# Performance work log

Hardware: AMD Instinct MI355X
Metric: run time of the kernel (lower is better)

Reference implementation:

```python
import jax, jax.numpy as jnp
import numpy as np

EPS = 1e-6
NUM_HEADS = 16

def _feature_map(x):
    # elu(x) + 1
    return jnp.where(x > 0, x + 1.0, jnp.exp(x))

def setup_inputs() -> dict:
    key = jax.random.key(0)
    ks = jax.random.split(key, 7)
    B, L, S, D = 4, 4096, 4096, 2048
    sc = 1.0 / np.sqrt(D)
    return {
        "query": jax.random.normal(ks[0], (B, L, D), jnp.float32),
        "kv": jax.random.normal(ks[1], (B, S, D), jnp.float32),
        "Wq": jax.random.normal(ks[2], (D, D), jnp.float32) * sc,
        "Wg": jax.random.normal(ks[3], (D, D), jnp.float32) * sc,
        "bg": jnp.ones((D,), jnp.float32),
        "Wkv": jax.random.normal(ks[4], (2 * D, D), jnp.float32) * sc,
        "Wo": jax.random.normal(ks[5], (D, D), jnp.float32) * sc,
    }

def reference(query, kv, Wq, Wg, bg, Wkv, Wo):
    B, L, D = query.shape
    S = kv.shape[1]
    H = NUM_HEADS
    hd = D // H
    q = query @ Wq.T                      # [B,L,D]
    gate = jax.nn.sigmoid(query @ Wg.T + bg)  # [B,L,D]
    kvp = kv @ Wkv.T                      # [B,S,2D]
    k, v = jnp.split(kvp, 2, axis=-1)
    # reshape to heads: [B,H,L,hd]
    q = _feature_map(q.reshape(B, L, H, hd).transpose(0, 2, 1, 3))
    k = _feature_map(k.reshape(B, S, H, hd).transpose(0, 2, 1, 3))
    v = v.reshape(B, S, H, hd).transpose(0, 2, 1, 3)
    kv_summary = jnp.einsum('bhsd,bhse->bhde', k, v)   # [B,H,hd,hd]
    k_sum = k.sum(axis=-2)                              # [B,H,hd]
    z = 1.0 / (jnp.einsum('bhld,bhd->bhl', q, k_sum)[..., None] + EPS)
    attn = jnp.einsum('bhld,bhde->bhle', q, kv_summary) * z  # [B,H,L,hd]
    attn = attn.transpose(0, 2, 1, 3).reshape(B, L, D)
    out = (attn * gate) @ Wo.T
    return out
```

## Files before the change

kernel.cpp:

```cpp
#include <hip/hip_runtime.h>

typedef __attribute__((ext_vector_type(8))) short bf16x8;
typedef __attribute__((ext_vector_type(4))) float f32x4;
typedef __attribute__((ext_vector_type(4))) unsigned int u32x4;

constexpr int L_ = 4096, S_ = 4096, D_ = 2048, H_ = 16, HD_ = 128;
constexpr int LDSS = 72;

__device__ __forceinline__ unsigned short f2bf(float f) {
    unsigned int u = __builtin_bit_cast(unsigned int, f);
    return (unsigned short)((u + 0x7fffu + ((u >> 16) & 1u)) >> 16);
}
__device__ __forceinline__ float bf2f(unsigned short h) {
    unsigned int u = ((unsigned int)h) << 16;
    return __builtin_bit_cast(float, u);
}
__device__ __forceinline__ unsigned long long pack4(float a, float b, float c, float d) {
    return (unsigned long long)f2bf(a) | ((unsigned long long)f2bf(b) << 16)
         | ((unsigned long long)f2bf(c) << 32) | ((unsigned long long)f2bf(d) << 48);
}
__device__ __forceinline__ float featmap(float x) {
    return x > 0.f ? x + 1.f : __expf(x);
}
__device__ __forceinline__ void gload16(const unsigned short* g, unsigned short* l) {
    __builtin_amdgcn_global_load_lds(
        (const __attribute__((address_space(1))) void*)g,
        (__attribute__((address_space(3))) void*)l, 16, 0, 0);
}

__global__ __launch_bounds__(256) void cvt_bf16(
    const float* __restrict__ in, unsigned short* __restrict__ out, int n8)
{
    const int stride = gridDim.x * 256;
    for (int i = blockIdx.x * 256 + threadIdx.x; i < n8; i += stride) {
        const float4 a = ((const float4*)in)[2 * i];
        const float4 b = ((const float4*)in)[2 * i + 1];
        unsigned long long* o = (unsigned long long*)&out[(size_t)i * 8];
        o[0] = pack4(a.x, a.y, a.z, a.w);
        o[1] = pack4(b.x, b.y, b.z, b.w);
    }
}

template<int MODE, int NBN>
__global__ __launch_bounds__(512, 2) void gemm256(
    const unsigned short* __restrict__ A, const unsigned short* __restrict__ B,
    unsigned short* __restrict__ C1, unsigned short* __restrict__ C2,
    float* __restrict__ Cf, const float* __restrict__ bias)
{
    __shared__ alignas(16) unsigned short lds[65536];
    const int tid = threadIdx.x;
    const int lane = tid & 63, w = tid >> 6;
    const int wr = w >> 2, wc = w & 3;
    const int lr = lane & 15;
    const int lk8 = (lane >> 4) * 8;
    const int rsw = (lr & 7) << 3;
    const int lsub = lane >> 3;
    const int scol = ((lane & 7) ^ lsub) * 8;

    const int nwg = gridDim.x;
    const int wg = blockIdx.x;
    const int swz = (wg & 7) * (nwg >> 3) + (wg >> 3);
    const int bm = swz / NBN, bn = swz % NBN;
    const int row0 = bm * 256, bcol = bn * 256;

    const unsigned short* Ap = A + (size_t)row0 * D_;
    const unsigned short* Bp = B + (size_t)bcol * D_;
    const int rA = w * 8 + lsub;
    const int rB = ((w * 8 + lsub) >> 5) * 64 + ((w * 8 + lsub) & 31);

    f32x4 acc[8][4] = {};
    bf16x8 av[2][4], bv[2][4];

#define STA(BUF, HH, KT) do { \
    const unsigned short* g_ = Ap + (size_t)((HH) * 64 + rA) * D_ + (KT) * 64 + scol; \
    unsigned short* l_ = &lds[(BUF) * 16384 + (HH) * 8192 + w * 512]; \
    gload16(g_, l_); gload16(g_ + (size_t)128 * D_, l_ + 4096); } while (0)

#define STB(BUF, HH, KT) do { \
    const unsigned short* g_ = Bp + (size_t)(rB + (HH) * 32) * D_ + (KT) * 64 + scol; \
    unsigned short* l_ = &lds[32768 + (BUF) * 16384 + (HH) * 8192 + w * 512]; \
    gload16(g_, l_); gload16(g_ + (size_t)128 * D_, l_ + 4096); } while (0)

#define RD_A(MQ, BUF) \
    _Pragma("unroll") for (int mi = 0; mi < 4; mi++) \
    _Pragma("unroll") for (int ks = 0; ks < 2; ks++) \
        av[ks][mi] = *(const bf16x8*)&lds[(BUF) * 16384 + (MQ) * 8192 \
            + (mi * 16 + lr + wr * 64) * 64 + ((ks * 32 + lk8) ^ rsw)];

#define RD_B(NQ, BUF) \
    _Pragma("unroll") for (int j = 0; j < 2; j++) \
    _Pragma("unroll") for (int ks = 0; ks < 2; ks++) \
        bv[ks][(NQ) * 2 + j] = *(const bf16x8*)&lds[32768 + (BUF) * 16384 + (NQ) * 8192 \
            + (j * 16 + lr + wc * 32) * 64 + ((ks * 32 + lk8) ^ rsw)];

#define MFMA_Q(MQ, NQ) \
    __builtin_amdgcn_s_setprio(1); \
    _Pragma("unroll") for (int mi = 0; mi < 4; mi++) \
    _Pragma("unroll") for (int j = 0; j < 2; j++) \
    _Pragma("unroll") for (int ks = 0; ks < 2; ks++) \
        acc[(MQ) * 4 + mi][(NQ) * 2 + j] = __builtin_amdgcn_mfma_f32_16x16x32_bf16( \
            av[ks][mi], bv[ks][(NQ) * 2 + j], acc[(MQ) * 4 + mi][(NQ) * 2 + j], 0, 0, 0); \
    __builtin_amdgcn_s_setprio(0);

#define BAR __builtin_amdgcn_s_barrier()
#define LGKM do { asm volatile("s_waitcnt lgkmcnt(0)" ::: "memory"); \
                  __builtin_amdgcn_sched_barrier(0); } while (0)
#define VM6 asm volatile("s_waitcnt vmcnt(6)" ::: "memory")
#define VM0 asm volatile("s_waitcnt vmcnt(0)" ::: "memory")

    STA(0, 0, 0); STB(0, 0, 0); STB(0, 1, 0); STA(0, 1, 0);
    STA(1, 0, 1); STB(1, 0, 1); STB(1, 1, 1);
    VM6;
    BAR;

    constexpr int NT = D_ / 64;
    for (int i = 0; i < NT / 2 - 1; i++) {
        const int T = 2 * i;
        RD_A(0, 0); RD_B(0, 0); STA(1, 1, T + 1);
        BAR; LGKM; MFMA_Q(0, 0); BAR;
        RD_B(1, 0); STA(0, 0, T + 2);
        BAR; LGKM; MFMA_Q(0, 1); BAR;
        RD_A(1, 0); STB(0, 0, T + 2);
        BAR; LGKM; MFMA_Q(1, 0); BAR;
        STB(0, 1, T + 2);
        VM6; BAR; MFMA_Q(1, 1); BAR;
        RD_A(0, 1); RD_B(0, 1); STA(0, 1, T + 2);
        BAR; LGKM; MFMA_Q(0, 0); BAR;
        RD_B(1, 1); STA(1, 0, T + 3);
        BAR; LGKM; MFMA_Q(0, 1); BAR;
        RD_A(1, 1); STB(1, 0, T + 3);
        BAR; LGKM; MFMA_Q(1, 0); BAR;
        STB(1, 1, T + 3);
        VM6; BAR; MFMA_Q(1, 1); BAR;
    }
    {
        RD_A(0, 0); RD_B(0, 0); STA(1, 1, NT - 1);
        BAR; LGKM; MFMA_Q(0, 0); BAR;
        RD_B(1, 0);
        BAR; LGKM; MFMA_Q(0, 1); BAR;
        RD_A(1, 0);
        BAR; LGKM; MFMA_Q(1, 0); BAR;
        VM0; BAR; MFMA_Q(1, 1); BAR;
        RD_A(0, 1); RD_B(0, 1);
        BAR; LGKM; MFMA_Q(0, 0); BAR;
        RD_B(1, 1);
        BAR; LGKM; MFMA_Q(0, 1); BAR;
        RD_A(1, 1);
        BAR; LGKM; MFMA_Q(1, 0); BAR;
        BAR; MFMA_Q(1, 1); BAR;
    }

    const int rb = (lane >> 4) * 4;
    const bool second = bn >= (NBN / 2);
    if (MODE == 1) {
        unsigned short* TT = lds;
        const int b = row0 >> 12;
        #pragma unroll
        for (int qd = 0; qd < 4; qd++) {
            const int sq = qd >> 1, dh = qd & 1;
            __syncthreads();
            if (wr == sq && (wc >> 1) == dh) {
                #pragma unroll
                for (int m = 0; m < 8; m++) {
                    #pragma unroll
                    for (int n = 0; n < 4; n++) {
                        float x0 = acc[m][n][0], x1 = acc[m][n][1];
                        float x2 = acc[m][n][2], x3 = acc[m][n][3];
                        if (!second) {
                            x0 = featmap(x0); x1 = featmap(x1);
                            x2 = featmap(x2); x3 = featmap(x3);
                        }
                        const int dcol = (wc & 1) * 64 + n * 16 + lr;
                        *(unsigned long long*)&TT[dcol * 136 + m * 16 + rb]
                            = pack4(x0, x1, x2, x3);
                    }
                }
            }
            __syncthreads();
            const int h2 = (bn & 7) * 2 + dh;
            const int s0 = (row0 + sq * 128) & (S_ - 1);
            unsigned short* dst = (second ? C2 : C1) + (size_t)(b * H_ + h2) * HD_ * S_;
            #pragma unroll
            for (int it = 0; it < 4; it++) {
                const int idx = it * 512 + tid;
                const int d = idx >> 4, sc2 = (idx & 15) * 8;
                *(u32x4*)&dst[(size_t)d * S_ + s0 + sc2] = *(const u32x4*)&TT[d * 136 + sc2];
            }
        }
        return;
    }
    #pragma unroll
    for (int m = 0; m < 8; m++) {
        #pragma unroll
        for (int n = 0; n < 4; n++) {
            #pragma unroll
            for (int r = 0; r < 4; r++) {
                const size_t gr = (size_t)(row0 + wr * 128 + m * 16 + rb + r);
                const int gc = bcol + wc * 64 + n * 16 + lr;
                float x = acc[m][n][r];
                if (MODE == 0) {
                    if (!second) {
                        C1[gr * D_ + gc] = f2bf(featmap(x));
                    } else {
                        const int gc2 = gc - D_;
                        float t = x + bias[gc2];
                        C2[gr * D_ + gc2] = f2bf(1.f / (1.f + __expf(-t)));
                    }
                } else {
                    Cf[gr * D_ + gc] = x;
                }
            }
        }
    }
#undef STA
#undef STB
#undef RD_A
#undef RD_B
#undef MFMA_Q
#undef BAR
#undef LGKM
#undef VM6
#undef VM0
}

__global__ __launch_bounds__(256) void kvsum_part(
    const unsigned short* __restrict__ kT, const unsigned short* __restrict__ vT,
    float* __restrict__ part, float* __restrict__ ksum_part)
{
    __shared__ unsigned short kA[HD_ * LDSS];
    __shared__ unsigned short vB[HD_ * LDSS];
    __shared__ float red[HD_ * 8];
    const int tid = threadIdx.x;
    const int cx = blockIdx.x, bh = blockIdx.y;
    const int lane = tid & 63, w = tid >> 6;
    const int wm = (w >> 1) * 64, wn = (w & 1) * 64;
    const int lr = lane & 15, lk = (lane >> 4) * 8;
    const unsigned short* kb = kT + (size_t)bh * HD_ * S_;
    const unsigned short* vb = vT + (size_t)bh * HD_ * S_;
    f32x4 acc[4][4] = {};
    float ksl[4] = {0.f, 0.f, 0.f, 0.f};
    const int chunk = S_ / 8;
    const int s_begin = cx * chunk;
    for (int s0 = s_begin; s0 < s_begin + chunk; s0 += 64) {
        #pragma unroll
        for (int i = 0; i < 4; i++) {
            int idx = tid + i * 256;
            int d = idx >> 3, sc = (idx & 7) * 8;
            u32x4 kk = *(const u32x4*)&kb[(size_t)d * S_ + s0 + sc];
            *(u32x4*)&kA[d * LDSS + sc] = kk;
            unsigned short t8[8];
            *(u32x4*)t8 = kk;
            float ss = 0.f;
            #pragma unroll
            for (int j = 0; j < 8; j++) ss += bf2f(t8[j]);
            ksl[i] += ss;
            *(u32x4*)&vB[d * LDSS + sc] = *(const u32x4*)&vb[(size_t)d * S_ + s0 + sc];
        }
        __syncthreads();
        #pragma unroll
        for (int ks = 0; ks < 64; ks += 32) {
            bf16x8 av[4], bv[4];
            #pragma unroll
            for (int mi = 0; mi < 4; mi++)
                av[mi] = *(const bf16x8*)&kA[(wm + mi * 16 + lr) * LDSS + ks + lk];
            #pragma unroll
            for (int ni = 0; ni < 4; ni++)
                bv[ni] = *(const bf16x8*)&vB[(wn + ni * 16 + lr) * LDSS + ks + lk];
            #pragma unroll
            for (int mi = 0; mi < 4; mi++)
                #pragma unroll
                for (int ni = 0; ni < 4; ni++)
                    acc[mi][ni] = __builtin_amdgcn_mfma_f32_16x16x32_bf16(
                        av[mi], bv[ni], acc[mi][ni], 0, 0, 0);
        }
        __syncthreads();
    }
    #pragma unroll
    for (int i = 0; i < 4; i++) red[((tid >> 3) + 32 * i) * 8 + (tid & 7)] = ksl[i];
    __syncthreads();
    if (tid < HD_) {
        float s = 0.f;
        #pragma unroll
        for (int j = 0; j < 8; j++) s += red[tid * 8 + j];
        ksum_part[(size_t)cx * (64 * HD_) + bh * HD_ + tid] = s;
    }
    const int rb = (lane >> 4) * 4;
    float* pp = part + ((size_t)cx * 64 + bh) * (HD_ * HD_);
    #pragma unroll
    for (int mi = 0; mi < 4; mi++)
        #pragma unroll
        for (int ni = 0; ni < 4; ni++)
            #pragma unroll
            for (int r = 0; r < 4; r++)
                pp[(wm + mi * 16 + rb + r) * HD_ + wn + ni * 16 + lr] = acc[mi][ni][r];
}

__global__ __launch_bounds__(256) void kvs_reduce(
    const float* __restrict__ part, unsigned short* __restrict__ kvsT,
    const float* __restrict__ ksum_part, float* __restrict__ ksum)
{
    const int idx = blockIdx.x * 256 + threadIdx.x;
    const int e = idx & 127, d2 = (idx >> 7) & 127, bh = idx >> 14;
    float s = 0.f;
    #pragma unroll
    for (int cx = 0; cx < 8; cx++)
        s += part[((size_t)cx * 64 + bh) * 16384 + d2 * 128 + e];
    kvsT[((size_t)bh * 128 + e) * 128 + d2] = f2bf(s);
    if (idx < 64 * 128) {
        float t = 0.f;
        #pragma unroll
        for (int cx = 0; cx < 8; cx++) t += ksum_part[cx * 8192 + idx];
        ksum[idx] = t;
    }
}

__global__ __launch_bounds__(256) void attn_kernel(
    const unsigned short* __restrict__ qf, const unsigned short* __restrict__ kvsT,
    const float* __restrict__ ksum, const unsigned short* __restrict__ gate,
    unsigned short* __restrict__ y)
{
    __shared__ unsigned short qs[128 * 136];
    __shared__ unsigned short bs[128 * LDSS];
    __shared__ float zl[128];
    const int tid = threadIdx.x;
    const int l0 = blockIdx.x * 128;
    const int h = blockIdx.y, b = blockIdx.z;
    const int bh = b * H_ + h;
    const int lane = tid & 63, w = tid >> 6;
    const int wm = (w >> 1) * 64, wn = (w & 1) * 64;
    const int lr = lane & 15, lk = (lane >> 4) * 8;
    const size_t qbase = (size_t)b * L_ * D_ + (size_t)h * HD_;
    #pragma unroll
    for (int i = 0; i < 8; i++) {
        int idx = tid + i * 256;
        int r = idx >> 4, c = (idx & 15) * 8;
        *(u32x4*)&qs[r * 136 + c] = *(const u32x4*)&qf[qbase + (size_t)(l0 + r) * D_ + c];
    }
    __syncthreads();
    if (tid < 128) {
        const float* kp = ksum + bh * HD_;
        float sden = 0.f;
        #pragma unroll 4
        for (int d2 = 0; d2 < HD_; d2++) sden += bf2f(qs[tid * 136 + d2]) * kp[d2];
        zl[tid] = 1.f / (sden + 1e-6f);
    }
    f32x4 acc[4][4] = {};
    for (int kc = 0; kc < 2; kc++) {
        #pragma unroll
        for (int i = 0; i < 4; i++) {
            int idx = tid + i * 256;
            int e = idx >> 3, dc = (idx & 7) * 8;
            *(u32x4*)&bs[e * LDSS + dc] =
                *(const u32x4*)&kvsT[((size_t)bh * 128 + e) * 128 + kc * 64 + dc];
        }
        __syncthreads();
        #pragma unroll
        for (int ks = 0; ks < 64; ks += 32) {
            bf16x8 av[4], bv[4];
            #pragma unroll
            for (int mi = 0; mi < 4; mi++)
                av[mi] = *(const bf16x8*)&qs[(wm + mi * 16 + lr) * 136 + kc * 64 + ks + lk];
            #pragma unroll
            for (int ni = 0; ni < 4; ni++)
                bv[ni] = *(const bf16x8*)&bs[(wn + ni * 16 + lr) * LDSS + ks + lk];
            #pragma unroll
            for (int mi = 0; mi < 4; mi++)
                #pragma unroll
                for (int ni = 0; ni < 4; ni++)
                    acc[mi][ni] = __builtin_amdgcn_mfma_f32_16x16x32_bf16(
                        av[mi], bv[ni], acc[mi][ni], 0, 0, 0);
        }
        __syncthreads();
    }
    const int rb = (lane >> 4) * 4;
    #pragma unroll
    for (int mi = 0; mi < 4; mi++) {
        #pragma unroll
        for (int ni = 0; ni < 4; ni++) {
            #pragma unroll
            for (int r = 0; r < 4; r++) {
                int ll = wm + mi * 16 + rb + r;
                int e = wn + ni * 16 + lr;
                float attn = acc[mi][ni][r] * zl[ll];
                float g = bf2f(gate[qbase + (size_t)(l0 + ll) * D_ + e]);
                y[qbase + (size_t)(l0 + ll) * D_ + e] = f2bf(attn * g);
            }
        }
    }
}

extern "C" void kernel_launch(void* const* d_in, const int* in_sizes, int n_in,
                              void* d_out, int out_size, void* d_ws, size_t ws_size,
                              hipStream_t stream)
{
    (void)in_sizes; (void)n_in; (void)out_size; (void)ws_size;
    const float* query = (const float*)d_in[0];
    const float* kv    = (const float*)d_in[1];
    const float* Wq    = (const float*)d_in[2];
    const float* Wg    = (const float*)d_in[3];
    const float* bg    = (const float*)d_in[4];
    const float* Wkv   = (const float*)d_in[5];
    const float* Wo    = (const float*)d_in[6];
    float* out = (float*)d_out;
    char* ws = (char*)d_ws;

    unsigned short* q_feat = (unsigned short*)(ws);
    unsigned short* gate   = (unsigned short*)(ws + 67108864);
    unsigned short* kTb    = (unsigned short*)(ws + 134217728);
    unsigned short* vTb    = (unsigned short*)(ws + 201326592);
    char* R = ws + 268435456;
    unsigned short* qbf    = (unsigned short*)(R);
    unsigned short* Wqg    = (unsigned short*)(R + 67108864);
    unsigned short* kvbf   = (unsigned short*)(R);
    unsigned short* Wkvb   = (unsigned short*)(R + 67108864);
    float* part            = (float*)(R);
    float* ksum_part       = (float*)(R + 33554432);
    float* ksum            = (float*)(R + 33816576);
    unsigned short* kvsT   = (unsigned short*)(R + 33849344);
    unsigned short* Wob    = (unsigned short*)(R + 83886080);
    unsigned short* ybuf   = kTb;

    dim3 blk(256, 1, 1);
    dim3 blk512(512, 1, 1);
    cvt_bf16<<<dim3(2048), blk, 0, stream>>>(query, qbf, 4194304);
    cvt_bf16<<<dim3(2048), blk, 0, stream>>>(Wq, Wqg, 524288);
    cvt_bf16<<<dim3(2048), blk, 0, stream>>>(Wg, Wqg + 4194304, 524288);
    cvt_bf16<<<dim3(2048), blk, 0, stream>>>(Wo, Wob, 524288);
    gemm256<0, 16><<<dim3(1024), blk512, 0, stream>>>(qbf, Wqg, q_feat, gate, nullptr, bg);
    cvt_bf16<<<dim3(2048), blk, 0, stream>>>(kv, kvbf, 4194304);
    cvt_bf16<<<dim3(2048), blk, 0, stream>>>(Wkv, Wkvb, 1048576);
    gemm256<1, 16><<<dim3(1024), blk512, 0, stream>>>(kvbf, Wkvb, kTb, vTb, nullptr, nullptr);
    kvsum_part<<<dim3(8, 64), blk, 0, stream>>>(kTb, vTb, part, ksum_part);
    kvs_reduce<<<dim3(4096), blk, 0, stream>>>(part, kvsT, ksum_part, ksum);
    attn_kernel<<<dim3(32, 16, 4), blk, 0, stream>>>(q_feat, kvsT, ksum, gate, ybuf);
    gemm256<2, 8><<<dim3(512), blk512, 0, stream>>>(ybuf, Wob, nullptr, nullptr, out, nullptr);
}
```

Measured before the change: 987.7 us.

## Restructure GEMM main loop into fewer barrier phases with prefetched B fragments

```diff
diff --git a/kernel.cpp b/kernel.cpp
--- a/kernel.cpp
+++ b/kernel.cpp
@@ -94,17 +94,16 @@
             + (j * 16 + lr + wc * 32) * 64 + ((ks * 32 + lk8) ^ rsw)];
 
 #define MFMA_Q(MQ, NQ) \
-    __builtin_amdgcn_s_setprio(1); \
     _Pragma("unroll") for (int mi = 0; mi < 4; mi++) \
     _Pragma("unroll") for (int j = 0; j < 2; j++) \
     _Pragma("unroll") for (int ks = 0; ks < 2; ks++) \
         acc[(MQ) * 4 + mi][(NQ) * 2 + j] = __builtin_amdgcn_mfma_f32_16x16x32_bf16( \
-            av[ks][mi], bv[ks][(NQ) * 2 + j], acc[(MQ) * 4 + mi][(NQ) * 2 + j], 0, 0, 0); \
-    __builtin_amdgcn_s_setprio(0);
-
+            av[ks][mi], bv[ks][(NQ) * 2 + j], acc[(MQ) * 4 + mi][(NQ) * 2 + j], 0, 0, 0);
+
+#define PRIO1 __builtin_amdgcn_s_setprio(1)
+#define PRIO0 __builtin_amdgcn_s_setprio(0)
+#define SB0 __builtin_amdgcn_sched_barrier(0)
 #define BAR __builtin_amdgcn_s_barrier()
-#define LGKM do { asm volatile("s_waitcnt lgkmcnt(0)" ::: "memory"); \
-                  __builtin_amdgcn_sched_barrier(0); } while (0)
 #define VM6 asm volatile("s_waitcnt vmcnt(6)" ::: "memory")
 #define VM0 asm volatile("s_waitcnt vmcnt(0)" ::: "memory")
 
@@ -112,42 +111,68 @@
     STA(1, 0, 1); STB(1, 0, 1); STB(1, 1, 1);
     VM6;
     BAR;
+    RD_B(0, 0);
 
     constexpr int NT = D_ / 64;
     for (int i = 0; i < NT / 2 - 1; i++) {
         const int T = 2 * i;
-        RD_A(0, 0); RD_B(0, 0); STA(1, 1, T + 1);
-        BAR; LGKM; MFMA_Q(0, 0); BAR;
-        RD_B(1, 0); STA(0, 0, T + 2);
-        BAR; LGKM; MFMA_Q(0, 1); BAR;
-        RD_A(1, 0); STB(0, 0, T + 2);
-        BAR; LGKM; MFMA_Q(1, 0); BAR;
+        RD_A(0, 0); RD_B(1, 0);
+        STA(1, 1, T + 1);
+        BAR;
+        PRIO1; MFMA_Q(0, 0); MFMA_Q(0, 1); PRIO0;
+        SB0;
+        BAR;
+        RD_A(1, 0);
+        STA(0, 0, T + 2);
+        STB(0, 0, T + 2);
         STB(0, 1, T + 2);
-        VM6; BAR; MFMA_Q(1, 1); BAR;
-        RD_A(0, 1); RD_B(0, 1); STA(0, 1, T + 2);
-        BAR; LGKM; MFMA_Q(0, 0); BAR;
-        RD_B(1, 1); STA(1, 0, T + 3);
-        BAR; LGKM; MFMA_Q(0, 1); BAR;
-        RD_A(1, 1); STB(1, 0, T + 3);
-        BAR; LGKM; MFMA_Q(1, 0); BAR;
+        VM6; BAR;
+        PRIO1; MFMA_Q(1, 0); PRIO0;
+        RD_B(0, 1);
+        PRIO1; MFMA_Q(1, 1); PRIO0;
+        SB0;
+        BAR;
+        RD_A(0, 1); RD_B(1, 1);
+        STA(0, 1, T + 2);
+        BAR;
+        PRIO1; MFMA_Q(0, 0); MFMA_Q(0, 1); PRIO0;
+        SB0;
+        BAR;
+        RD_A(1, 1);
+        STA(1, 0, T + 3);
+        STB(1, 0, T + 3);
         STB(1, 1, T + 3);
-        VM6; BAR; MFMA_Q(1, 1); BAR;
+        VM6; BAR;
+        PRIO1; MFMA_Q(1, 0); PRIO0;
+        RD_B(0, 0);
+        PRIO1; MFMA_Q(1, 1); PRIO0;
+        SB0;
+        BAR;
     }
     {
-        RD_A(0, 0); RD_B(0, 0); STA(1, 1, NT - 1);
-        BAR; LGKM; MFMA_Q(0, 0); BAR;
-        RD_B(1, 0);
-        BAR; LGKM; MFMA_Q(0, 1); BAR;
+        RD_A(0, 0); RD_B(1, 0);
+        STA(1, 1, NT - 1);
+        BAR;
+        PRIO1; MFMA_Q(0, 0); MFMA_Q(0, 1); PRIO0;
+        SB0;
+        BAR;
         RD_A(1, 0);
-        BAR; LGKM; MFMA_Q(1, 0); BAR;
-        VM0; BAR; MFMA_Q(1, 1); BAR;
-        RD_A(0, 1); RD_B(0, 1);
-        BAR; LGKM; MFMA_Q(0, 0); BAR;
-        RD_B(1, 1);
-        BAR; LGKM; MFMA_Q(0, 1); BAR;
+        VM0; BAR;
+        PRIO1; MFMA_Q(1, 0); PRIO0;
+        RD_B(0, 1);
+        PRIO1; MFMA_Q(1, 1); PRIO0;
+        SB0;
+        BAR;
+        RD_A(0, 1); RD_B(1, 1);
+        BAR;
+        PRIO1; MFMA_Q(0, 0); MFMA_Q(0, 1); PRIO0;
+        SB0;
+        BAR;
         RD_A(1, 1);
-        BAR; LGKM; MFMA_Q(1, 0); BAR;
-        BAR; MFMA_Q(1, 1); BAR;
+        BAR;
+        PRIO1; MFMA_Q(1, 0); MFMA_Q(1, 1); PRIO0;
+        SB0;
+        BAR;
     }
 
     const int rb = (lane >> 4) * 4;
@@ -217,8 +242,10 @@
 #undef RD_A
 #undef RD_B
 #undef MFMA_Q
+#undef PRIO1
+#undef PRIO0
+#undef SB0
 #undef BAR
-#undef LGKM
 #undef VM6
 #undef VM0
 }
```

Result: no change. 986.7 us (-0.1%).

## Double-buffer GEMM fragment registers to overlap LDS reads with MFMA

Applied to the files above, without the earlier changes.

```diff
diff --git a/kernel.cpp b/kernel.cpp
--- a/kernel.cpp
+++ b/kernel.cpp
@@ -69,7 +69,8 @@
     const int rB = ((w * 8 + lsub) >> 5) * 64 + ((w * 8 + lsub) & 31);
 
     f32x4 acc[8][4] = {};
-    bf16x8 av[2][4], bv[2][4];
+    bf16x8 avx[2][4], avy[2][4];
+    bf16x8 bva[2][2], bvb[2][2];
 
 #define STA(BUF, HH, KT) do { \
     const unsigned short* g_ = Ap + (size_t)((HH) * 64 + rA) * D_ + (KT) * 64 + scol; \
@@ -81,73 +82,74 @@
     unsigned short* l_ = &lds[32768 + (BUF) * 16384 + (HH) * 8192 + w * 512]; \
     gload16(g_, l_); gload16(g_ + (size_t)128 * D_, l_ + 4096); } while (0)
 
-#define RD_A(MQ, BUF) \
+#define RD_As(DST, MQ, BUF) \
     _Pragma("unroll") for (int mi = 0; mi < 4; mi++) \
     _Pragma("unroll") for (int ks = 0; ks < 2; ks++) \
-        av[ks][mi] = *(const bf16x8*)&lds[(BUF) * 16384 + (MQ) * 8192 \
+        DST[ks][mi] = *(const bf16x8*)&lds[(BUF) * 16384 + (MQ) * 8192 \
             + (mi * 16 + lr + wr * 64) * 64 + ((ks * 32 + lk8) ^ rsw)];
 
-#define RD_B(NQ, BUF) \
+#define RD_Bs(DST, NQ, BUF) \
     _Pragma("unroll") for (int j = 0; j < 2; j++) \
     _Pragma("unroll") for (int ks = 0; ks < 2; ks++) \
-        bv[ks][(NQ) * 2 + j] = *(const bf16x8*)&lds[32768 + (BUF) * 16384 + (NQ) * 8192 \
+        DST[ks][j] = *(const bf16x8*)&lds[32768 + (BUF) * 16384 + (NQ) * 8192 \
             + (j * 16 + lr + wc * 32) * 64 + ((ks * 32 + lk8) ^ rsw)];
 
-#define MFMA_Q(MQ, NQ) \
-    __builtin_amdgcn_s_setprio(1); \
+#define MFMA_G(MQ, NQ, AV, BV) \
     _Pragma("unroll") for (int mi = 0; mi < 4; mi++) \
     _Pragma("unroll") for (int j = 0; j < 2; j++) \
     _Pragma("unroll") for (int ks = 0; ks < 2; ks++) \
         acc[(MQ) * 4 + mi][(NQ) * 2 + j] = __builtin_amdgcn_mfma_f32_16x16x32_bf16( \
-            av[ks][mi], bv[ks][(NQ) * 2 + j], acc[(MQ) * 4 + mi][(NQ) * 2 + j], 0, 0, 0); \
-    __builtin_amdgcn_s_setprio(0);
-
+            AV[ks][mi], BV[ks][j], acc[(MQ) * 4 + mi][(NQ) * 2 + j], 0, 0, 0);
+
+#define PRIO1 __builtin_amdgcn_s_setprio(1)
+#define PRIO0 __builtin_amdgcn_s_setprio(0)
 #define BAR __builtin_amdgcn_s_barrier()
-#define LGKM do { asm volatile("s_waitcnt lgkmcnt(0)" ::: "memory"); \
-                  __builtin_amdgcn_sched_barrier(0); } while (0)
-#define VM6 asm volatile("s_waitcnt vmcnt(6)" ::: "memory")
+#define LG0 asm volatile("s_waitcnt lgkmcnt(0)" ::: "memory")
+#define VM4 asm volatile("s_waitcnt vmcnt(4)" ::: "memory")
 #define VM0 asm volatile("s_waitcnt vmcnt(0)" ::: "memory")
 
-    STA(0, 0, 0); STB(0, 0, 0); STB(0, 1, 0); STA(0, 1, 0);
-    STA(1, 0, 1); STB(1, 0, 1); STB(1, 1, 1);
-    VM6;
-    BAR;
+    STA(0, 0, 0); STB(0, 0, 0); STA(0, 1, 0); STB(0, 1, 0);
+    STA(1, 0, 1); STB(1, 0, 1); STA(1, 1, 1); STB(1, 1, 1);
+    VM0; BAR;
+    RD_As(avx, 0, 0);
+    RD_Bs(bva, 0, 0);
+    LG0;
 
     constexpr int NT = D_ / 64;
     for (int i = 0; i < NT / 2 - 1; i++) {
-        const int T = 2 * i;
-        RD_A(0, 0); RD_B(0, 0); STA(1, 1, T + 1);
-        BAR; LGKM; MFMA_Q(0, 0); BAR;
-        RD_B(1, 0); STA(0, 0, T + 2);
-        BAR; LGKM; MFMA_Q(0, 1); BAR;
-        RD_A(1, 0); STB(0, 0, T + 2);
-        BAR; LGKM; MFMA_Q(1, 0); BAR;
-        STB(0, 1, T + 2);
-        VM6; BAR; MFMA_Q(1, 1); BAR;
-        RD_A(0, 1); RD_B(0, 1); STA(0, 1, T + 2);
-        BAR; LGKM; MFMA_Q(0, 0); BAR;
-        RD_B(1, 1); STA(1, 0, T + 3);
-        BAR; LGKM; MFMA_Q(0, 1); BAR;
-        RD_A(1, 1); STB(1, 0, T + 3);
-        BAR; LGKM; MFMA_Q(1, 0); BAR;
-        STB(1, 1, T + 3);
-        VM6; BAR; MFMA_Q(1, 1); BAR;
+        const int t2 = 2 * i + 2, t3 = 2 * i + 3;
+        RD_Bs(bvb, 1, 0); STA(0, 0, t2);
+        PRIO1; MFMA_G(0, 0, avx, bva); PRIO0; LG0; BAR;
+        RD_As(avy, 1, 0); STB(0, 0, t2);
+        PRIO1; MFMA_G(0, 1, avx, bvb); PRIO0; LG0; VM4; BAR;
+        RD_As(avx, 0, 1); STA(0, 1, t2);
+        PRIO1; MFMA_G(1, 1, avy, bvb); PRIO0; LG0; BAR;
+        RD_Bs(bvb, 0, 1); STB(0, 1, t2);
+        PRIO1; MFMA_G(1, 0, avy, bva); PRIO0; LG0; BAR;
+        RD_Bs(bva, 1, 1); STA(1, 0, t3);
+        PRIO1; MFMA_G(0, 0, avx, bvb); PRIO0; LG0; BAR;
+        RD_As(avy, 1, 1); STB(1, 0, t3);
+        PRIO1; MFMA_G(0, 1, avx, bva); PRIO0; LG0; VM4; BAR;
+        RD_As(avx, 0, 0); STA(1, 1, t3);
+        PRIO1; MFMA_G(1, 1, avy, bva); PRIO0; LG0; BAR;
+        RD_Bs(bva, 0, 0); STB(1, 1, t3);
+        PRIO1; MFMA_G(1, 0, avy, bvb); PRIO0; LG0; BAR;
     }
     {
-        RD_A(0, 0); RD_B(0, 0); STA(1, 1, NT - 1);
-        BAR; LGKM; MFMA_Q(0, 0); BAR;
-        RD_B(1, 0);
-        BAR; LGKM; MFMA_Q(0, 1); BAR;
-        RD_A(1, 0);
-        BAR; LGKM; MFMA_Q(1, 0); BAR;
-        VM0; BAR; MFMA_Q(1, 1); BAR;
-        RD_A(0, 1); RD_B(0, 1);
-        BAR; LGKM; MFMA_Q(0, 0); BAR;
-        RD_B(1, 1);
-        BAR; LGKM; MFMA_Q(0, 1); BAR;
-        RD_A(1, 1);
-        BAR; LGKM; MFMA_Q(1, 0); BAR;
-        BAR; MFMA_Q(1, 1); BAR;
+        RD_Bs(bvb, 1, 0);
+        PRIO1; MFMA_G(0, 0, avx, bva); PRIO0; LG0; BAR;
+        RD_As(avy, 1, 0);
+        PRIO1; MFMA_G(0, 1, avx, bvb); PRIO0; LG0; VM0; BAR;
+        RD_As(avx, 0, 1);
+        PRIO1; MFMA_G(1, 1, avy, bvb); PRIO0; LG0; BAR;
+        RD_Bs(bvb, 0, 1);
+        PRIO1; MFMA_G(1, 0, avy, bva); PRIO0; LG0; BAR;
+        RD_Bs(bva, 1, 1);
+        PRIO1; MFMA_G(0, 0, avx, bvb); PRIO0; LG0; BAR;
+        RD_As(avy, 1, 1);
+        PRIO1; MFMA_G(0, 1, avx, bva); PRIO0; LG0; BAR;
+        PRIO1; MFMA_G(1, 1, avy, bva); PRIO0; BAR;
+        PRIO1; MFMA_G(1, 0, avy, bvb); PRIO0; BAR;
     }
 
     const int rb = (lane >> 4) * 4;
@@ -214,12 +216,14 @@
     }
 #undef STA
 #undef STB
-#undef RD_A
-#undef RD_B
-#undef MFMA_Q
+#undef RD_As
+#undef RD_Bs
+#undef MFMA_G
+#undef PRIO1
+#undef PRIO0
 #undef BAR
-#undef LGKM
-#undef VM6
+#undef LG0
+#undef VM4
 #undef VM0
 }
 
```

Result: slower. 1.223 ms (+23.8%).
